# Kernel tuning notes

Measured on AMD Instinct MI355X. Metric: run time of the kernel, lower is better.

## Reference

```python
import jax, jax.numpy as jnp
from jax import lax
import numpy as np

# (cin, cout, kernel, pad) for the 18 convs (funs 1,3,5,6,7,9,10,11,13..17,19..23)
CONVS = [(3,32,3,0),(32,64,3,0),(64,128,3,1),(128,64,1,0),(64,128,3,1),
         (128,256,3,1),(256,128,1,0),(128,256,3,0),(256,512,3,1),(512,256,1,0),
         (256,512,3,1),(512,256,1,0),(256,512,3,0),(512,256,3,1),(256,128,1,0),
         (128,64,3,1),(64,32,1,0),(32,6,3,1)]
# maxpool(2,2) after conv index (1-based) -> pool padding (torch pads with -inf, floor mode)
POOL_AFTER = {1: 1, 2: 1, 5: 0, 8: 1, 13: 1}
GT = (0.567, 0.469, 0.206, 0.53)  # hardcoded ground-truth box (cx, cy, w, h), normalized


def _backbone(x, ws, bs):
    for i, (w, b) in enumerate(zip(ws, bs), 1):
        pad = CONVS[i - 1][3]
        x = lax.conv_general_dilated(
            x, w, (1, 1), [(pad, pad), (pad, pad)],
            dimension_numbers=("NCHW", "OIHW", "NCHW")) + b[None, :, None, None]
        if i in POOL_AFTER:
            p = POOL_AFTER[i]
            x = lax.reduce_window(
                x, -jnp.inf, lax.max, (1, 1, 2, 2), (1, 1, 2, 2),
                [(0, 0), (0, 0), (p, p), (p, p)])
    return x


def _head(x):
    # torch: x.transpose(1,3) on [B,6,H,W] -> [B,W,H,6]; j indexes W, k indexes H
    xt = jnp.transpose(x, (0, 3, 2, 1))
    B, W, H, _ = xt.shape
    j = jnp.arange(W, dtype=xt.dtype)[None, :, None]  # [1,W,1]
    k = jnp.arange(H, dtype=xt.dtype)[None, None, :]  # [1,1,H]
    px = (j + xt[..., 2]) / W
    py = (k + xt[..., 3]) / H
    pw = jnp.exp(xt[..., 4]) / W
    ph = jnp.exp(xt[..., 5]) / H
    # center-format IoU against the single gt box (detached mask, as in torch via float())
    iw = jnp.clip(jnp.minimum(px + pw * 0.5, GT[0] + GT[2] * 0.5)
                  - jnp.maximum(px - pw * 0.5, GT[0] - GT[2] * 0.5), 0.0)
    ih = jnp.clip(jnp.minimum(py + ph * 0.5, GT[1] + GT[3] * 0.5)
                  - jnp.maximum(py - ph * 0.5, GT[1] - GT[3] * 0.5), 0.0)
    inter = iw * ih
    iou = inter / (pw * ph + GT[2] * GT[3] - inter)
    iou = lax.stop_gradient(iou)
    tx = GT[0] * W - j          # [1,W,1]
    ty = GT[1] * H - k          # [1,1,H]
    tw = np.log(GT[2] * W).astype(np.float32)
    th = np.log(GT[3] * H).astype(np.float32)
    l1 = (jnp.abs(tx - xt[..., 2]) + jnp.abs(ty - xt[..., 3])
          + jnp.abs(tw - xt[..., 4]) + jnp.abs(th - xt[..., 5]))
    loss = jnp.sum(jnp.where(iou > 0.5, l1, 0.0)).reshape(1)
    return xt, loss


def setup_inputs() -> dict:
    key = jax.random.key(0)
    keys = jax.random.split(key, 1 + 2 * len(CONVS))
    d = {"x": jax.random.normal(keys[0], (16, 3, 416, 416), jnp.float32)}
    for i, (cin, cout, ks, _) in enumerate(CONVS, 1):
        fan_in = cin * ks * ks
        d[f"w{i}"] = jax.random.normal(keys[2 * i - 1], (cout, cin, ks, ks), jnp.float32) / np.sqrt(fan_in)
        d[f"b{i}"] = jax.random.normal(keys[2 * i], (cout,), jnp.float32) * 0.01
    return d


def reference(x, w1, b1, w2, b2, w3, b3, w4, b4, w5, b5, w6, b6, w7, b7, w8, b8,
              w9, b9, w10, b10, w11, b11, w12, b12, w13, b13, w14, b14, w15, b15,
              w16, b16, w17, b17, w18, b18):
    ws = [w1, w2, w3, w4, w5, w6, w7, w8, w9, w10, w11, w12, w13, w14, w15, w16, w17, w18]
    bs = [b1, b2, b3, b4, b5, b6, b7, b8, b9, b10, b11, b12, b13, b14, b15, b16, b17, b18]
    feat = _backbone(x, ws, bs)
    xt, loss = _head(feat)
    return (xt, loss)
```

## Files before the change

### kernel.cpp

```cpp
#include <hip/hip_runtime.h>
#include <math.h>

typedef short v8s __attribute__((ext_vector_type(8)));
typedef float v4f __attribute__((ext_vector_type(4)));

template<int K, int COT, bool POOL, bool MASK, bool SWAP>
__global__ __launch_bounds__(256) void conv_fused(
    const float* __restrict__ in, const float* __restrict__ wgt,
    const float* __restrict__ bias, float* __restrict__ out,
    int B, int Cin, int Hin, int Win,
    int Hc, int Wc, int Hout, int Wout,
    int Cout, int cpad, int ppad,
    int inPS, int inRS, int inOfs, int outPS, int outRS, int outOfs)
{
    constexpr int NPY = POOL ? 2 : 1;
    constexpr int PS  = K + NPY - 1;
    const int spatial = Hout * Wout;
    const int idx = (SWAP ? blockIdx.y : blockIdx.x) * blockDim.x + threadIdx.x;
    const int cog = SWAP ? blockIdx.x : blockIdx.y;
    const int total = B * spatial;
    if (idx >= total) return;
    const int b  = idx / spatial;
    const int sp = idx - b * spatial;
    const int oy = sp / Wout;
    const int ox = sp - oy * Wout;
    const int co0 = cog * COT;

    const int cy0 = POOL ? (2 * oy - ppad) : oy;
    const int cx0 = POOL ? (2 * ox - ppad) : ox;
    const int iy0 = cy0 - cpad;
    const int ix0 = cx0 - cpad;

    bool my[PS], mx[PS];
#pragma unroll
    for (int i = 0; i < PS; i++) {
        my[i] = !MASK || ((unsigned)(iy0 + i) < (unsigned)Hin);
        mx[i] = !MASK || ((unsigned)(ix0 + i) < (unsigned)Win);
    }

    float acc[COT][NPY * NPY];
#pragma unroll
    for (int c = 0; c < COT; c++)
#pragma unroll
        for (int p = 0; p < NPY * NPY; p++) acc[c][p] = 0.f;

    const float* inB = in + inOfs + (size_t)b * Cin * inPS;
    const long wBase  = (long)co0 * Cin * K * K;

    for (int ci = 0; ci < Cin; ci++) {
        const float* ip = inB + (size_t)ci * inPS;
        float patch[PS][PS];
#pragma unroll
        for (int py = 0; py < PS; py++) {
#pragma unroll
            for (int px = 0; px < PS; px++) {
                float v = 0.f;
                if (my[py] && mx[px]) v = ip[(iy0 + py) * inRS + (ix0 + px)];
                patch[py][px] = v;
            }
        }
        const float* wp = wgt + wBase + (long)ci * K * K;
#pragma unroll
        for (int c = 0; c < COT; c++) {
#pragma unroll
            for (int kh = 0; kh < K; kh++)
#pragma unroll
            for (int kw = 0; kw < K; kw++) {
                const float wv = wp[(long)c * Cin * K * K + kh * K + kw];
#pragma unroll
                for (int dy = 0; dy < NPY; dy++)
#pragma unroll
                for (int dx = 0; dx < NPY; dx++)
                    acc[c][dy * NPY + dx] = fmaf(wv, patch[dy + kh][dx + kw],
                                                 acc[c][dy * NPY + dx]);
            }
        }
    }

#pragma unroll
    for (int c = 0; c < COT; c++) {
        float v;
        if (POOL) {
            v = -INFINITY;
#pragma unroll
            for (int dy = 0; dy < NPY; dy++)
#pragma unroll
            for (int dx = 0; dx < NPY; dx++) {
                const int cy = cy0 + dy, cx = cx0 + dx;
                if ((unsigned)cy < (unsigned)Hc && (unsigned)cx < (unsigned)Wc)
                    v = fmaxf(v, acc[c][dy * NPY + dx]);
            }
        } else {
            v = acc[c][0];
        }
        v += bias[co0 + c];
        out[outOfs + (size_t)(b * Cout + co0 + c) * outPS + oy * outRS + ox] = v;
    }
}

__global__ __launch_bounds__(256) void ring_zero(
    float* __restrict__ buf, int planes, int H, int W)
{
    int Wp = W + 2, Hp = H + 2;
    int ringlen = 2 * Wp + 2 * H;
    int t = blockIdx.x * 256 + threadIdx.x;
    if (t >= planes * ringlen) return;
    int p = t / ringlen, r = t - p * ringlen;
    float* pl = buf + (size_t)p * Hp * Wp;
    int idx;
    if (r < Wp) idx = r;
    else if (r < 2 * Wp) idx = (Hp - 1) * Wp + (r - Wp);
    else { int rr = r - 2 * Wp; int row = 1 + (rr >> 1); idx = row * Wp + ((rr & 1) ? (Wp - 1) : 0); }
    pl[idx] = 0.f;
}

__device__ __forceinline__ unsigned short f2bf_rne(float x) {
    unsigned u = __float_as_uint(x);
    return (unsigned short)((u + 0x7fffu + ((u >> 16) & 1u)) >> 16);
}
__device__ __forceinline__ float bf2f(unsigned short h) {
    return __uint_as_float(((unsigned)h) << 16);
}

__global__ __launch_bounds__(256) void prepack(
    const float* __restrict__ w, unsigned short* __restrict__ hi,
    unsigned short* __restrict__ lo, int cout, int kdim, int nkb)
{
    int t = blockIdx.x * 256 + threadIdx.x;
    if (t >= cout * kdim) return;
    int co = t / kdim, k = t - co * kdim;
    int cb = co >> 4, m = co & 15, kb = k >> 5, kk = k & 31;
    int lane = ((kk >> 3) << 4) | m, j = kk & 7;
    long dst = ((long)(cb * nkb + kb) << 9) + lane * 8 + j;
    float x = w[t];
    unsigned short h = f2bf_rne(x);
    hi[dst] = h;
    lo[dst] = f2bf_rne(x - bf2f(h));
}

template<int MT, int KS, bool SPLIT>
__global__ __launch_bounds__(256) void conv_mfma(
    const float* __restrict__ in, const unsigned short* __restrict__ whi,
    const unsigned short* __restrict__ wlo, const float* __restrict__ bias,
    float* __restrict__ out, int Cin, int inHWp, int inWp, int Hc, int Wc,
    int Cout, int pad, int b0, int nb, int nkbTot, int nkbPer, int Mpad,
    int outHWp, int outWp)
{
    const int HW = Hc * Wc;
    const int M = nb * HW;
    const int tid = threadIdx.x;
    const int lane = tid & 63;
    const int wv = tid >> 6;
    const int spBase = blockIdx.x * 64;
    const int kb0 = SPLIT ? blockIdx.z * nkbPer : 0;
    const int kb1 = SPLIT ? kb0 + nkbPer : nkbTot;

    __shared__ unsigned short P[2][5120];

    const int spo = lane >> 2;
    const int kp  = (tid & 3) + 4 * wv;

    int jbase[4];
#pragma unroll
    for (int j = 0; j < 4; ++j) {
        int sp = spBase + spo + 16 * j;
        int q = sp < M ? sp : M - 1;
        int b = q / HW; int r = q - b * HW;
        int soy = r / Wc, sox = r - soy * Wc;
        jbase[j] = (b0 + b) * Cin * inHWp + (soy + 1) * inWp + (sox + 1);
    }

    int ci[2], r9[2], koff[2];
#pragma unroll
    for (int m = 0; m < 2; ++m) {
        int k = kb0 * 32 + 2 * kp + m;
        if (KS == 3) {
            ci[m] = k / 9; r9[m] = k - 9 * ci[m];
            int d3 = (r9[m] >= 3) + (r9[m] >= 6);
            koff[m] = ci[m] * inHWp + (d3 - pad) * inWp + (r9[m] - 3 * d3 - pad);
        } else { ci[m] = k; koff[m] = k * inHWp; }
    }

    float rv[8];
#define STAGE()                                                                \
    {                                                                          \
        _Pragma("unroll")                                                      \
        for (int m = 0; m < 2; ++m)                                            \
        _Pragma("unroll")                                                      \
        for (int j = 0; j < 4; ++j)                                            \
            rv[m * 4 + j] = in[jbase[j] + koff[m]];                            \
    }
#define ADVANCE()                                                              \
    {                                                                          \
        _Pragma("unroll")                                                      \
        for (int m = 0; m < 2; ++m) {                                          \
            if (KS == 3) {                                                     \
                r9[m] += 5; int c = r9[m] >= 9; r9[m] -= c ? 9 : 0;            \
                ci[m] += 3 + c;                                                \
                int d3 = (r9[m] >= 3) + (r9[m] >= 6);                          \
                koff[m] = ci[m] * inHWp + (d3 - pad) * inWp                    \
                        + (r9[m] - 3 * d3 - pad);                              \
            } else { koff[m] += 32 * inHWp; }                                  \
        }                                                                      \
    }

    STAGE();

    const int g0 = blockIdx.y * (MT * 4) + wv * MT;
    const unsigned short* whp[MT];
    const unsigned short* wlp[MT];
#pragma unroll
    for (int mt = 0; mt < MT; ++mt) {
        size_t base = (((size_t)(g0 + mt) * nkbTot + kb0) << 9) + lane * 8;
        whp[mt] = whi + base; wlp[mt] = wlo + base;
    }

    v8s WHa[MT], WHb[MT];
#pragma unroll
    for (int mt = 0; mt < MT; ++mt) { WHa[mt] = *(const v8s*)whp[mt]; whp[mt] += 512; }

    v4f acc[MT][4];
    {
        v4f z = {0.f, 0.f, 0.f, 0.f};
#pragma unroll
        for (int mt = 0; mt < MT; ++mt)
#pragma unroll
            for (int nt = 0; nt < 4; ++nt) acc[mt][nt] = z;
    }

#define CHUNK(WC, WN)                                                          \
    {                                                                          \
        unsigned short* Pl = P[kb & 1];                                        \
        _Pragma("unroll")                                                      \
        for (int j = 0; j < 4; ++j) {                                          \
            unsigned vb0 = __float_as_uint(rv[j]);                             \
            unsigned vb1 = __float_as_uint(rv[4 + j]);                         \
            unsigned hiP = (vb0 >> 16) | (vb1 & 0xffff0000u);                  \
            float r0 = rv[j]     - __uint_as_float(vb0 & 0xffff0000u);         \
            float r1 = rv[4 + j] - __uint_as_float(vb1 & 0xffff0000u);         \
            unsigned loP = (__float_as_uint(r0) >> 16)                         \
                         | (__float_as_uint(r1) & 0xffff0000u);                \
            int a = (spo + 16 * j) * 40 + 2 * kp;                              \
            *(unsigned*)(Pl + a) = hiP;                                        \
            *(unsigned*)(Pl + 2560 + a) = loP;                                 \
        }                                                                      \
        __syncthreads();                                                       \
        v8s wl_[MT];                                                           \
        _Pragma("unroll")                                                      \
        for (int mt = 0; mt < MT; ++mt) {                                      \
            wl_[mt] = *(const v8s*)wlp[mt]; wlp[mt] += 512;                    \
        }                                                                      \
        if (kb + 1 < kb1) {                                                    \
            _Pragma("unroll")                                                  \
            for (int mt = 0; mt < MT; ++mt) {                                  \
                WN[mt] = *(const v8s*)whp[mt]; whp[mt] += 512;                 \
            }                                                                  \
            ADVANCE(); STAGE();                                                \
        }                                                                      \
        v8s phr[4];                                                            \
        _Pragma("unroll")                                                      \
        for (int nt = 0; nt < 4; ++nt) {                                       \
            int ro = (nt * 16 + (lane & 15)) * 40 + (lane >> 4) * 8;           \
            phr[nt] = *(const v8s*)(Pl + ro);                                  \
            v8s plr = *(const v8s*)(Pl + 2560 + ro);                           \
            _Pragma("unroll")                                                  \
            for (int mt = 0; mt < MT; ++mt) {                                  \
                acc[mt][nt] = __builtin_amdgcn_mfma_f32_16x16x32_bf16(         \
                    WC[mt], phr[nt], acc[mt][nt], 0, 0, 0);                    \
                acc[mt][nt] = __builtin_amdgcn_mfma_f32_16x16x32_bf16(         \
                    WC[mt], plr, acc[mt][nt], 0, 0, 0);                        \
            }                                                                  \
        }                                                                      \
        _Pragma("unroll")                                                      \
        for (int nt = 0; nt < 4; ++nt)                                         \
        _Pragma("unroll")                                                      \
        for (int mt = 0; mt < MT; ++mt)                                        \
            acc[mt][nt] = __builtin_amdgcn_mfma_f32_16x16x32_bf16(             \
                wl_[mt], phr[nt], acc[mt][nt], 0, 0, 0);                       \
    }

    int kb = kb0;
    for (;;) {
        CHUNK(WHa, WHb);
        if (++kb >= kb1) break;
        CHUNK(WHb, WHa);
        if (++kb >= kb1) break;
    }
#undef CHUNK
#undef STAGE
#undef ADVANCE

    const int qrow = (lane >> 4) * 4;
    if (SPLIT) {
        float* pz = out + (size_t)blockIdx.z * Cout * Mpad;
#pragma unroll
        for (int mt = 0; mt < MT; ++mt) {
            int co = (g0 + mt) * 16 + qrow;
#pragma unroll
            for (int nt = 0; nt < 4; ++nt) {
                int sp = spBase + nt * 16 + (lane & 15);
                if (sp < M) {
#pragma unroll
                    for (int r = 0; r < 4; ++r)
                        pz[(size_t)(co + r) * Mpad + sp] = acc[mt][nt][r];
                }
            }
        }
    } else {
#pragma unroll
        for (int mt = 0; mt < MT; ++mt) {
            int co = (g0 + mt) * 16 + qrow;
            float bsv[4];
#pragma unroll
            for (int r = 0; r < 4; ++r) bsv[r] = bias[co + r];
#pragma unroll
            for (int nt = 0; nt < 4; ++nt) {
                int sp = spBase + nt * 16 + (lane & 15);
                if (sp < M) {
                    int b = sp / HW, rsp = sp - b * HW;
                    int y = rsp / Wc, xx = rsp - y * Wc;
                    float* op = out + (size_t)(b * Cout + co) * outHWp
                              + (size_t)(y + 1) * outWp + (xx + 1);
#pragma unroll
                    for (int r = 0; r < 4; ++r)
                        op[(size_t)r * outHWp] = acc[mt][nt][r] + bsv[r];
                }
            }
        }
    }
}

__global__ __launch_bounds__(256) void sk_reduce(
    const float* __restrict__ part, const float* __restrict__ bias,
    float* __restrict__ out, int Cout, int HW, int Wc, int M, int Mpad, int SK,
    int outHWp, int outWp)
{
    int t = blockIdx.x * 256 + threadIdx.x;
    if (t >= Cout * M) return;
    int co = t / M, m = t - co * M;
    float s = bias[co];
    for (int k = 0; k < SK; ++k)
        s += part[((size_t)k * Cout + co) * Mpad + m];
    int b = m / HW, rsp = m - b * HW;
    int y = rsp / Wc, xx = rsp - y * Wc;
    out[(size_t)(b * Cout + co) * outHWp + (size_t)(y + 1) * outWp + (xx + 1)] = s;
}

__global__ __launch_bounds__(256) void maxpool_k(
    const float* __restrict__ in, float* __restrict__ out,
    int Hc, int Wc, int Hp, int Wp, int p, int total,
    int inHWp, int inWp, int outHWp, int outWp)
{
    int t = blockIdx.x * 256 + threadIdx.x;
    if (t >= total) return;
    int wp2 = Hp * Wp;
    int bc = t / wp2; int r = t - bc * wp2;
    int y = r / Wp, xx = r - y * Wp;
    int y0 = 2 * y - p, x0 = 2 * xx - p;
    const float* ip = in + (size_t)bc * inHWp;
    float v = -INFINITY;
#pragma unroll
    for (int dy = 0; dy < 2; ++dy)
#pragma unroll
    for (int dx = 0; dx < 2; ++dx) {
        int yy = y0 + dy, xc = x0 + dx;
        if ((unsigned)yy < (unsigned)Hc && (unsigned)xc < (unsigned)Wc)
            v = fmaxf(v, ip[(yy + 1) * inWp + (xc + 1)]);
    }
    out[(size_t)bc * outHWp + (size_t)(y + 1) * outWp + (xx + 1)] = v;
}

__global__ __launch_bounds__(1024) void head_kernel(
    const float* __restrict__ x, float* __restrict__ out, int B)
{
    const int W = 13, H = 13;
    const float gx = 0.567f, gy = 0.469f, gw = 0.206f, gh = 0.53f;
    const int tid = threadIdx.x;
    const int total = B * W * H;
    float lsum = 0.f;
    for (int i = tid; i < total; i += blockDim.x) {
        const int b = i / (W * H);
        const int r = i - b * W * H;
        const int j = r / H;
        const int k = r - j * H;
        float v[6];
#pragma unroll
        for (int c = 0; c < 6; c++) {
            v[c] = x[((b * 6 + c) * H + k) * W + j];
            out[((b * W + j) * H + k) * 6 + c] = v[c];
        }
        const float px = (j + v[2]) / (float)W;
        const float py = (k + v[3]) / (float)H;
        const float pw = expf(v[4]) / (float)W;
        const float ph = expf(v[5]) / (float)H;
        float iw = fminf(px + pw * 0.5f, gx + gw * 0.5f)
                 - fmaxf(px - pw * 0.5f, gx - gw * 0.5f);
        iw = fmaxf(iw, 0.f);
        float ih = fminf(py + ph * 0.5f, gy + gh * 0.5f)
                 - fmaxf(py - ph * 0.5f, gy - gh * 0.5f);
        ih = fmaxf(ih, 0.f);
        const float inter = iw * ih;
        const float iou = inter / (pw * ph + gw * gh - inter);
        const float tx = gx * W - (float)j;
        const float ty = gy * H - (float)k;
        const float tw = logf(gw * W);
        const float th = logf(gh * H);
        const float l1 = fabsf(tx - v[2]) + fabsf(ty - v[3])
                       + fabsf(tw - v[4]) + fabsf(th - v[5]);
        if (iou > 0.5f) lsum += l1;
    }
    __shared__ float red[1024];
    red[tid] = lsum;
    __syncthreads();
    for (int s = blockDim.x / 2; s > 0; s >>= 1) {
        if (tid < s) red[tid] += red[tid + s];
        __syncthreads();
    }
    if (tid == 0) out[total * 6] = red[0];
}

extern "C" void kernel_launch(void* const* d_in, const int* in_sizes, int n_in,
                              void* d_out, int out_size, void* d_ws, size_t ws_size,
                              hipStream_t stream)
{
    (void)in_sizes; (void)n_in; (void)out_size;
    const float* x = (const float*)d_in[0];
    const int B = 16;
    const size_t MB = 1024 * 1024;
    char* ws = (char*)d_ws;
    float* bufA = (float*)ws;
    float* bufB = (float*)(ws + 93 * MB);
    unsigned short* WHI = (unsigned short*)(ws + 141 * MB);
    unsigned short* WLO = (unsigned short*)(ws + 153 * MB);
    char* TEMP = ws + 165 * MB;
    const bool gemmOK = ws_size >= 166 * MB;
    const size_t tempAvail = ws_size > 165 * MB ? ws_size - 165 * MB : 0;

    static const struct { int cin, cout, ks, cpad, pool, ppad; } L[18] = {
        {3,  32, 3, 0, 1, 1}, {32, 64, 3, 0, 1, 1}, {64, 128, 3, 1, 0, 0},
        {128, 64, 1, 0, 0, 0}, {64, 128, 3, 1, 1, 0}, {128, 256, 3, 1, 0, 0},
        {256, 128, 1, 0, 0, 0}, {128, 256, 3, 0, 1, 1}, {256, 512, 3, 1, 0, 0},
        {512, 256, 1, 0, 0, 0}, {256, 512, 3, 1, 0, 0}, {512, 256, 1, 0, 0, 0},
        {256, 512, 3, 0, 1, 1}, {512, 256, 3, 1, 0, 0}, {256, 128, 1, 0, 0, 0},
        {128, 64, 3, 1, 0, 0}, {64, 32, 1, 0, 0, 0}, {32, 6, 3, 1, 0, 0}
    };
    static const bool RING[18] = {0,1,0,1,1,0,0,1,0,1,0,0,1,0,1,0,1,0};

    if (gemmOK) {
        size_t off = 0;
        for (int i = 1; i <= 15; ++i) {
            int kdim = L[i].cin * L[i].ks * L[i].ks;
            int n = L[i].cout * kdim;
            prepack<<<(n + 255) / 256, 256, 0, stream>>>(
                (const float*)d_in[2 * i + 1], WHI + off, WLO + off,
                L[i].cout, kdim, kdim / 32);
            off += (size_t)n;
        }
    }

    const float* cur = x;
    int Hin = 416, Win = 416;
    size_t woff = 0;

    for (int i = 0; i < 18; ++i) {
        const auto& l = L[i];
        const int Hc = Hin + 2 * l.cpad - l.ks + 1;
        const int Wc = Win + 2 * l.cpad - l.ks + 1;
        const int Hout = l.pool ? (Hc + 2 * l.ppad - 2) / 2 + 1 : Hc;
        const int Wout = l.pool ? (Wc + 2 * l.ppad - 2) / 2 + 1 : Wc;
        float* dst = (i % 2 == 0) ? bufA : bufB;
        const float* w  = (const float*)d_in[2 * i + 1];
        const float* bb = (const float*)d_in[2 * i + 2];
        const int kdim = l.cin * l.ks * l.ks;
        const int nkb = kdim / 32;

        const int inRS  = (i == 0) ? Win : (Win + 2);
        const int inPS  = (i == 0) ? Hin * Win : (Hin + 2) * (Win + 2);
        const int inOfs = (i == 0) ? 0 : (inRS + 1);
        const bool outPad = (i != 17);
        const int outRS  = outPad ? (Wout + 2) : Wout;
        const int outPS  = outPad ? (Hout + 2) * (Wout + 2) : Hout * Wout;
        const int outOfs = outPad ? (outRS + 1) : 0;
        const int tRS = Wc + 2, tPS = (Hc + 2) * (Wc + 2);

        if (RING[i]) {
            int planes = B * l.cout;
            int ringlen = 2 * (Wout + 2) + 2 * Hout;
            ring_zero<<<(planes * ringlen + 255) / 256, 256, 0, stream>>>(
                dst, planes, Hout, Wout);
        }

        int nb = 16;
        if (l.pool) {
            size_t perImg = (size_t)l.cout * tPS * 4;
            while (nb && perImg * (size_t)nb > tempAvail) nb >>= 1;
        }
        const bool useG = gemmOK && i >= 1 && i <= 15 && (!l.pool || nb >= 1);

        if (useG) {
            for (int b0 = 0; b0 < B; b0 += nb) {
                const int M = nb * Hc * Wc;
                const int gx = (M + 63) / 64;
                const int Mpad = gx * 64;
                int MTv = (l.cout >= 256) ? 4 : (l.cout >= 128 ? 2 : 1);
                int gy = l.cout / (MTv * 64);
                int SK = 1;
                if (!l.pool) {
                    while ((long)gx * gy * SK < 512 && SK < 16 &&
                           nkb % (SK * 2) == 0 &&
                           (size_t)(SK * 2) * l.cout * Mpad * 4 <= tempAvail)
                        SK *= 2;
                } else {
                    while (MTv > 1 && (long)gx * gy < 512) {
                        MTv >>= 1; gy = l.cout / (MTv * 64);
                    }
                }
                const int nkbPer = nkb / SK;
                float* gout = l.pool ? (float*)TEMP : (SK > 1 ? (float*)TEMP : dst);
                const int gHWp = l.pool ? tPS : (SK > 1 ? 0 : outPS);
                const int gWp  = l.pool ? tRS : (SK > 1 ? 0 : outRS);
                dim3 gr(gx, gy, SK);
#define GL(MTC, KSC, SPL)                                                      \
                conv_mfma<MTC, KSC, SPL><<<gr, 256, 0, stream>>>(              \
                    cur, WHI + woff, WLO + woff, bb, gout, l.cin, inPS, inRS,  \
                    Hc, Wc, l.cout, l.cpad, b0, nb, nkb, nkbPer, Mpad,         \
                    gHWp, gWp)
#define G2(MTC, KSC) do { if (SK > 1) GL(MTC, KSC, true); else GL(MTC, KSC, false); } while (0)
                if (MTv == 4)      { if (l.ks == 3) G2(4, 3); else G2(4, 1); }
                else if (MTv == 2) { if (l.ks == 3) G2(2, 3); else G2(2, 1); }
                else               { if (l.ks == 3) G2(1, 3); else G2(1, 1); }
#undef G2
#undef GL
                if (SK > 1) {
                    int tot = l.cout * M;
                    sk_reduce<<<(tot + 255) / 256, 256, 0, stream>>>(
                        (const float*)TEMP, bb, dst, l.cout, Hc * Wc, Wc, M,
                        Mpad, SK, outPS, outRS);
                }
                if (l.pool) {
                    int total = nb * l.cout * Hout * Wout;
                    maxpool_k<<<(total + 255) / 256, 256, 0, stream>>>(
                        (const float*)TEMP,
                        dst + (size_t)b0 * l.cout * outPS,
                        Hc, Wc, Hout, Wout, l.ppad, total, tPS, tRS, outPS, outRS);
                }
            }
        } else {
            const int spatial = Hout * Wout;
#define FL(KK, CC, PP, MM, SW)                                                 \
            conv_fused<KK, CC, PP, MM, SW><<<                                  \
                SW ? dim3(l.cout / CC, (B * spatial + 255) / 256)              \
                   : dim3((B * spatial + 255) / 256, l.cout / CC),             \
                256, 0, stream>>>(                                             \
                cur, w, bb, dst, B, l.cin, Hin, Win, Hc, Wc, Hout, Wout,       \
                l.cout, l.cpad, l.ppad, inPS, inRS, inOfs, outPS, outRS, outOfs)
            if (i == 0)                           FL(3, 8, true, true, true);
            else if (i == 16)                     FL(1, 8, false, false, false);
            else if (i == 17)                     FL(3, 6, false, false, false);
            else if (l.pool)                      FL(3, 4, true, true, false);
            else if (l.ks == 3)                   FL(3, 8, false, true, false);
            else                                  FL(1, 8, false, true, false);
#undef FL
        }

        if (i >= 1 && i <= 15) woff += (size_t)l.cout * kdim;
        cur = dst;
        Hin = Hout;
        Win = Wout;
    }

    head_kernel<<<1, 1024, 0, stream>>>(cur, (float*)d_out, B);
}
```

Before: 1.650 ms.

## Add triple-buffered deep-prefetch MFMA conv path and drop pooled-layer MT reduction

Adds a DEEP variant of the MFMA implicit-GEMM conv that triple-buffers the LDS input tile, keeps two global input stages in flight, and preloads both hi and lo weight fragments one chunk ahead. It is selected when the grid is small (at most 700 blocks), where latency hiding rather than occupancy is expected to dominate. The non-deep path is simplified so it loads weights after the barrier with no weight prefetch. The heuristic that shrank MT for pooled layers to raise block count is removed, so pooled layers now keep larger tiles. The deep path uses more LDS and registers per block, which can lower occupancy.

```diff
diff --git a/kernel.cpp b/kernel.cpp
--- a/kernel.cpp
+++ b/kernel.cpp
@@ -138,7 +138,7 @@
     lo[dst] = f2bf_rne(x - bf2f(h));
 }
 
-template<int MT, int KS, bool SPLIT>
+template<int MT, int KS, bool SPLIT, bool DEEP>
 __global__ __launch_bounds__(256) void conv_mfma(
     const float* __restrict__ in, const unsigned short* __restrict__ whi,
     const unsigned short* __restrict__ wlo, const float* __restrict__ bias,
@@ -154,8 +154,9 @@
     const int spBase = blockIdx.x * 64;
     const int kb0 = SPLIT ? blockIdx.z * nkbPer : 0;
     const int kb1 = SPLIT ? kb0 + nkbPer : nkbTot;
-
-    __shared__ unsigned short P[2][5120];
+    const int n = kb1 - kb0;
+
+    __shared__ unsigned short P[DEEP ? 3 : 2][5120];
 
     const int spo = lane >> 2;
     const int kp  = (tid & 3) + 4 * wv;
@@ -181,30 +182,69 @@
         } else { ci[m] = k; koff[m] = k * inHWp; }
     }
 
-    float rv[8];
-#define STAGE()                                                                \
+#define STAGE(RV)                                                              \
     {                                                                          \
         _Pragma("unroll")                                                      \
         for (int m = 0; m < 2; ++m)                                            \
         _Pragma("unroll")                                                      \
         for (int j = 0; j < 4; ++j)                                            \
-            rv[m * 4 + j] = in[jbase[j] + koff[m]];                            \
-    }
-#define ADVANCE()                                                              \
+            RV[m * 4 + j] = in[jbase[j] + koff[m]];                            \
+    }
+#define ADV()                                                                  \
     {                                                                          \
         _Pragma("unroll")                                                      \
         for (int m = 0; m < 2; ++m) {                                          \
             if (KS == 3) {                                                     \
-                r9[m] += 5; int c = r9[m] >= 9; r9[m] -= c ? 9 : 0;            \
-                ci[m] += 3 + c;                                                \
+                r9[m] += 5; int c_ = r9[m] >= 9; r9[m] -= c_ ? 9 : 0;          \
+                ci[m] += 3 + c_;                                               \
                 int d3 = (r9[m] >= 3) + (r9[m] >= 6);                          \
                 koff[m] = ci[m] * inHWp + (d3 - pad) * inWp                    \
                         + (r9[m] - 3 * d3 - pad);                              \
             } else { koff[m] += 32 * inHWp; }                                  \
         }                                                                      \
     }
-
-    STAGE();
+#define LDSW(PL, RV)                                                           \
+    {                                                                          \
+        _Pragma("unroll")                                                      \
+        for (int j = 0; j < 4; ++j) {                                          \
+            unsigned vb0 = __float_as_uint(RV[j]);                             \
+            unsigned vb1 = __float_as_uint(RV[4 + j]);                         \
+            unsigned hiP = (vb0 >> 16) | (vb1 & 0xffff0000u);                  \
+            float r0 = RV[j]     - __uint_as_float(vb0 & 0xffff0000u);         \
+            float r1 = RV[4 + j] - __uint_as_float(vb1 & 0xffff0000u);         \
+            unsigned loP = (__float_as_uint(r0) >> 16)                         \
+                         | (__float_as_uint(r1) & 0xffff0000u);                \
+            int a = (spo + 16 * j) * 40 + 2 * kp;                              \
+            *(unsigned*)((PL) + a) = hiP;                                      \
+            *(unsigned*)((PL) + 2560 + a) = loP;                               \
+        }                                                                      \
+    }
+#define MFMAPH(PL, WH, WL)                                                     \
+    {                                                                          \
+        _Pragma("unroll")                                                      \
+        for (int nt = 0; nt < 4; ++nt) {                                       \
+            int ro = (nt * 16 + (lane & 15)) * 40 + (lane >> 4) * 8;           \
+            v8s ph = *(const v8s*)((PL) + ro);                                 \
+            v8s pl = *(const v8s*)((PL) + 2560 + ro);                          \
+            _Pragma("unroll")                                                  \
+            for (int mt = 0; mt < MT; ++mt) {                                  \
+                acc[mt][nt] = __builtin_amdgcn_mfma_f32_16x16x32_bf16(         \
+                    WH[mt], ph, acc[mt][nt], 0, 0, 0);                         \
+                acc[mt][nt] = __builtin_amdgcn_mfma_f32_16x16x32_bf16(         \
+                    WH[mt], pl, acc[mt][nt], 0, 0, 0);                         \
+                acc[mt][nt] = __builtin_amdgcn_mfma_f32_16x16x32_bf16(         \
+                    WL[mt], ph, acc[mt][nt], 0, 0, 0);                         \
+            }                                                                  \
+        }                                                                      \
+    }
+#define WLOADTO(WH, WL)                                                        \
+    {                                                                          \
+        _Pragma("unroll")                                                      \
+        for (int mt = 0; mt < MT; ++mt) {                                      \
+            WH[mt] = *(const v8s*)whp[mt]; whp[mt] += 512;                     \
+            WL[mt] = *(const v8s*)wlp[mt]; wlp[mt] += 512;                     \
+        }                                                                      \
+    }
 
     const int g0 = blockIdx.y * (MT * 4) + wv * MT;
     const unsigned short* whp[MT];
@@ -215,10 +255,6 @@
         whp[mt] = whi + base; wlp[mt] = wlo + base;
     }
 
-    v8s WHa[MT], WHb[MT];
-#pragma unroll
-    for (int mt = 0; mt < MT; ++mt) { WHa[mt] = *(const v8s*)whp[mt]; whp[mt] += 512; }
-
     v4f acc[MT][4];
     {
         v4f z = {0.f, 0.f, 0.f, 0.f};
@@ -228,67 +264,53 @@
             for (int nt = 0; nt < 4; ++nt) acc[mt][nt] = z;
     }
 
-#define CHUNK(WC, WN)                                                          \
-    {                                                                          \
-        unsigned short* Pl = P[kb & 1];                                        \
-        _Pragma("unroll")                                                      \
-        for (int j = 0; j < 4; ++j) {                                          \
-            unsigned vb0 = __float_as_uint(rv[j]);                             \
-            unsigned vb1 = __float_as_uint(rv[4 + j]);                         \
-            unsigned hiP = (vb0 >> 16) | (vb1 & 0xffff0000u);                  \
-            float r0 = rv[j]     - __uint_as_float(vb0 & 0xffff0000u);         \
-            float r1 = rv[4 + j] - __uint_as_float(vb1 & 0xffff0000u);         \
-            unsigned loP = (__float_as_uint(r0) >> 16)                         \
-                         | (__float_as_uint(r1) & 0xffff0000u);                \
-            int a = (spo + 16 * j) * 40 + 2 * kp;                              \
-            *(unsigned*)(Pl + a) = hiP;                                        \
-            *(unsigned*)(Pl + 2560 + a) = loP;                                 \
-        }                                                                      \
-        __syncthreads();                                                       \
-        v8s wl_[MT];                                                           \
-        _Pragma("unroll")                                                      \
-        for (int mt = 0; mt < MT; ++mt) {                                      \
-            wl_[mt] = *(const v8s*)wlp[mt]; wlp[mt] += 512;                    \
-        }                                                                      \
-        if (kb + 1 < kb1) {                                                    \
-            _Pragma("unroll")                                                  \
-            for (int mt = 0; mt < MT; ++mt) {                                  \
-                WN[mt] = *(const v8s*)whp[mt]; whp[mt] += 512;                 \
-            }                                                                  \
-            ADVANCE(); STAGE();                                                \
-        }                                                                      \
-        v8s phr[4];                                                            \
-        _Pragma("unroll")                                                      \
-        for (int nt = 0; nt < 4; ++nt) {                                       \
-            int ro = (nt * 16 + (lane & 15)) * 40 + (lane >> 4) * 8;           \
-            phr[nt] = *(const v8s*)(Pl + ro);                                  \
-            v8s plr = *(const v8s*)(Pl + 2560 + ro);                           \
-            _Pragma("unroll")                                                  \
-            for (int mt = 0; mt < MT; ++mt) {                                  \
-                acc[mt][nt] = __builtin_amdgcn_mfma_f32_16x16x32_bf16(         \
-                    WC[mt], phr[nt], acc[mt][nt], 0, 0, 0);                    \
-                acc[mt][nt] = __builtin_amdgcn_mfma_f32_16x16x32_bf16(         \
-                    WC[mt], plr, acc[mt][nt], 0, 0, 0);                        \
-            }                                                                  \
-        }                                                                      \
-        _Pragma("unroll")                                                      \
-        for (int nt = 0; nt < 4; ++nt)                                         \
-        _Pragma("unroll")                                                      \
-        for (int mt = 0; mt < MT; ++mt)                                        \
-            acc[mt][nt] = __builtin_amdgcn_mfma_f32_16x16x32_bf16(             \
-                wl_[mt], phr[nt], acc[mt][nt], 0, 0, 0);                       \
-    }
-
-    int kb = kb0;
-    for (;;) {
-        CHUNK(WHa, WHb);
-        if (++kb >= kb1) break;
-        CHUNK(WHb, WHa);
-        if (++kb >= kb1) break;
-    }
-#undef CHUNK
+    if (DEEP) {
+        float rv0[8], rv1[8];
+        STAGE(rv0); ADV();
+        if (n > 1) { STAGE(rv1); ADV(); }
+        LDSW(&P[0][0], rv0);
+        if (n > 2) { STAGE(rv0); ADV(); }
+        v8s whA[MT], wlA[MT], whB[MT], wlB[MT];
+        WLOADTO(whA, wlA);
+        __syncthreads();
+        int br = 0, bw = 1;
+#define ITER(C, WC, LC, WN, LN, RVX)                                           \
+        {                                                                      \
+            unsigned short* Pw = &P[bw][0];                                    \
+            if ((C) + 1 < n) LDSW(Pw, RVX);                                    \
+            if ((C) + 3 < n) { STAGE(RVX); ADV(); }                            \
+            if ((C) + 1 < n) { WLOADTO(WN, LN); }                              \
+            __syncthreads();                                                   \
+            unsigned short* Pr = &P[br][0];                                    \
+            MFMAPH(Pr, WC, LC);                                                \
+            br = bw; bw = (bw == 2) ? 0 : bw + 1;                              \
+        }
+        int c = 0;
+        for (;;) {
+            ITER(c, whA, wlA, whB, wlB, rv1);
+            if (++c >= n) break;
+            ITER(c, whB, wlB, whA, wlA, rv0);
+            if (++c >= n) break;
+        }
+#undef ITER
+    } else {
+        float rv[8];
+        STAGE(rv);
+        for (int cc = 0; cc < n; ++cc) {
+            unsigned short* Pl = &P[cc & 1][0];
+            LDSW(Pl, rv);
+            __syncthreads();
+            v8s wh[MT], wl[MT];
+            WLOADTO(wh, wl);
+            if (cc + 1 < n) { ADV(); STAGE(rv); }
+            MFMAPH(Pl, wh, wl);
+        }
+    }
 #undef STAGE
-#undef ADVANCE
+#undef ADV
+#undef LDSW
+#undef MFMAPH
+#undef WLOADTO
 
     const int qrow = (lane >> 4) * 4;
     if (SPLIT) {
@@ -508,28 +530,33 @@
                 if (!l.pool) {
                     while ((long)gx * gy * SK < 512 && SK < 16 &&
                            nkb % (SK * 2) == 0 &&
-                           (size_t)(SK * 2) * l.cout * Mpad * 4 <= tempAvail)
+                           (size_t)(SK * 2) * l.cout * (size_t)Mpad * 4 <= tempAvail)
                         SK *= 2;
-                } else {
-                    while (MTv > 1 && (long)gx * gy < 512) {
-                        MTv >>= 1; gy = l.cout / (MTv * 64);
-                    }
                 }
+                const bool deep = ((long)gx * gy * SK <= 700);
                 const int nkbPer = nkb / SK;
                 float* gout = l.pool ? (float*)TEMP : (SK > 1 ? (float*)TEMP : dst);
                 const int gHWp = l.pool ? tPS : (SK > 1 ? 0 : outPS);
                 const int gWp  = l.pool ? tRS : (SK > 1 ? 0 : outRS);
                 dim3 gr(gx, gy, SK);
-#define GL(MTC, KSC, SPL)                                                      \
-                conv_mfma<MTC, KSC, SPL><<<gr, 256, 0, stream>>>(              \
+#define GL(MTC, KSC, SPL, DP)                                                  \
+                conv_mfma<MTC, KSC, SPL, DP><<<gr, 256, 0, stream>>>(          \
                     cur, WHI + woff, WLO + woff, bb, gout, l.cin, inPS, inRS,  \
                     Hc, Wc, l.cout, l.cpad, b0, nb, nkb, nkbPer, Mpad,         \
                     gHWp, gWp)
-#define G2(MTC, KSC) do { if (SK > 1) GL(MTC, KSC, true); else GL(MTC, KSC, false); } while (0)
-                if (MTv == 4)      { if (l.ks == 3) G2(4, 3); else G2(4, 1); }
-                else if (MTv == 2) { if (l.ks == 3) G2(2, 3); else G2(2, 1); }
-                else               { if (l.ks == 3) G2(1, 3); else G2(1, 1); }
-#undef G2
+#define G3(MTC, KSC)                                                           \
+                do {                                                           \
+                    if (SK > 1) { if (deep) GL(MTC, KSC, true, true);          \
+                                  else      GL(MTC, KSC, true, false); }       \
+                    else        { if (deep) GL(MTC, KSC, false, true);         \
+                                  else      GL(MTC, KSC, false, false); }      \
+                } while (0)
+#define G4(MTC) do { if (l.ks == 3) G3(MTC, 3); else G3(MTC, 1); } while (0)
+                if (MTv == 4) G4(4);
+                else if (MTv == 2) G4(2);
+                else G4(1);
+#undef G4
+#undef G3
 #undef GL
                 if (SK > 1) {
                     int tot = l.cout * M;
```

Result: faster. 1.552 ms (-5.9%).
